# Kernel optimization log

Hardware: AMD Instinct MI355X
Metric: run time of the kernel (lower is better)

Reference implementation:

```python
import jax, jax.numpy as jnp
import numpy as np

EPS_BN = 1e-5
EPS_COS = 1e-8
M_BINS = 10


def _bn(x, g, b):
    # eval-mode BatchNorm2d with running_mean=0, running_var=1
    s = g / jnp.sqrt(1.0 + EPS_BN)
    return x * s[None, :, None, None] + b[None, :, None, None]


def _dw(x, w, pad, dil):
    # depthwise conv, x [B,C,H,W], w [C,1,kh,kw]
    return jax.lax.conv_general_dilated(
        x, w, window_strides=(1, 1), padding=pad, rhs_dilation=dil,
        dimension_numbers=('NCHW', 'OIHW', 'NCHW'),
        feature_group_count=x.shape[1])


def setup_inputs() -> dict:
    key = jax.random.key(0)
    ks = jax.random.split(key, 20)
    B, INP, OUP, H, W = 16, 64, 64, 128, 128
    f32 = jnp.float32
    d = {}
    d['x'] = jax.random.normal(ks[0], (B, INP, H, W), f32)
    d['w_conv1'] = jax.random.normal(ks[1], (OUP, INP), f32) * 0.05
    d['pr_w1'] = jax.random.normal(ks[2], (OUP, 1, 1, 5), f32) * 0.2
    d['pr_w2'] = jax.random.normal(ks[3], (OUP, 1, 5, 1), f32) * 0.2
    d['pr_w3'] = jax.random.normal(ks[4], (OUP, 1, 1, 5), f32) * 0.2
    d['pr_w4'] = jax.random.normal(ks[5], (OUP, 1, 5, 1), f32) * 0.2
    d['pr_gamma'] = 1.0 + 0.1 * jax.random.normal(ks[6], (5, OUP), f32)
    d['pr_beta'] = 0.1 * jax.random.normal(ks[7], (5, OUP), f32)
    d['bn1_g'] = 1.0 + 0.1 * jax.random.normal(ks[8], (OUP,), f32)
    d['bn1_b'] = 0.1 * jax.random.normal(ks[9], (OUP,), f32)
    d['bn2_g'] = 1.0 + 0.1 * jax.random.normal(ks[10], (OUP,), f32)
    d['bn2_b'] = 0.1 * jax.random.normal(ks[11], (OUP,), f32)
    d['fc1_w'] = jax.random.normal(ks[12], (OUP, 2), f32) * 0.5
    d['fc1_b'] = 0.1 * jax.random.normal(ks[13], (OUP,), f32)
    d['phi1_w'] = jax.random.normal(ks[14], (OUP, OUP), f32) * 0.1
    d['phi1_b'] = 0.01 * jax.random.normal(ks[15], (OUP,), f32)
    d['phi2_w'] = jax.random.normal(ks[16], (OUP, OUP), f32) * 0.1
    d['phi2_b'] = 0.01 * jax.random.normal(ks[17], (OUP,), f32)
    d['phi3_w'] = jax.random.normal(ks[18], (OUP, OUP), f32) * 0.1
    d['phi3_b'] = 0.01 * jax.random.normal(ks[19], (OUP,), f32)
    d['w_conv2'] = jax.random.normal(jax.random.fold_in(key, 99), (OUP, 1), f32) * 0.1
    return d


def reference(x, w_conv1, pr_w1, pr_w2, pr_w3, pr_w4, pr_gamma, pr_beta,
              bn1_g, bn1_b, bn2_g, bn2_b, fc1_w, fc1_b,
              phi1_w, phi1_b, phi2_w, phi2_b, phi3_w, phi3_b, w_conv2):
    B, C, H, W = x.shape
    M = M_BINS
    OUP = w_conv1.shape[0]
    # conv1 (1x1) + Position_reinforcement branch
    x_c = jnp.einsum('oc,bchw->bohw', w_conv1, x)
    h = _bn(x_c, pr_gamma[0], pr_beta[0])
    h = _dw(h, pr_w1, ((0, 0), (2, 2)), (1, 1))
    h = _bn(h, pr_gamma[1], pr_beta[1])
    h = _dw(h, pr_w2, ((2, 2), (0, 0)), (1, 1))
    h = _bn(h, pr_gamma[2], pr_beta[2])
    h = _dw(h, pr_w3, ((0, 0), (4, 4)), (2, 2))
    h = _bn(h, pr_gamma[3], pr_beta[3])
    h = _dw(h, pr_w4, ((4, 4), (0, 0)), (2, 2))
    x_center = _bn(h, pr_gamma[4], pr_beta[4])
    # cosine similarity of each pixel feature with the global-avg feature
    g = jnp.mean(x, axis=(2, 3), keepdims=True)             # [B,C,1,1]
    num = jnp.sum(g * x, axis=1)                            # [B,H,W]
    gn = jnp.maximum(jnp.sqrt(jnp.sum(g * g, axis=1)), EPS_COS)
    xn = jnp.maximum(jnp.sqrt(jnp.sum(x * x, axis=1)), EPS_COS)
    S = num / (gn * xn)                                     # [B,H,W]
    Sf = S.reshape(B, H * W)
    # torch casts min/max with float() -> detached constants
    mn = jax.lax.stop_gradient(jnp.min(Sf, axis=1))
    mx = jax.lax.stop_gradient(jnp.max(Sf, axis=1))
    t = jnp.arange(M, dtype=x.dtype) / (M - 1)
    levels = mn[:, None] + (mx - mn)[:, None] * t[None, :]  # [B,M]
    diff = jnp.abs(levels[:, None, :] - Sf[:, :, None])     # [B,HW,M] soft bins
    V = jnp.where(diff < 0.5 / M, 1.0 - diff, jnp.zeros((), x.dtype))
    colsum = jnp.sum(V, axis=1)                             # [B,M]
    # torch normalizes by V.sum() while only columns 0..j are filled -> cumsum
    denom = jnp.cumsum(colsum, axis=1)
    Ch = jnp.stack([colsum / denom, levels], axis=-1)       # [B,M,2]
    Cf = Ch.reshape(-1, 2) @ fc1_w.T + fc1_b                # [B*M,OUP]
    Cq = Cf.reshape(B, OUP, M)                              # raw view as in torch
    p1 = jnp.einsum('oc,bcm->bom', phi1_w, Cq) + phi1_b[None, :, None]
    p2 = jnp.einsum('oc,bcm->bom', phi2_w, Cq) + phi2_b[None, :, None]
    X = jax.nn.softmax(jnp.einsum('bcm,bcn->bmn', p1, p2), axis=-1)  # [B,M,M]
    p3 = jnp.einsum('oc,bcm->bom', phi3_w, Cq) + phi3_b[None, :, None]
    Lp = jnp.einsum('bcm,bmn->bcn', p3, X)                  # [B,OUP,M]
    Vr = V.reshape(B, M, H * W)                             # raw view as in torch
    R = jnp.einsum('bcm,bmk->bck', Lp, Vr).reshape(B, OUP, H, W)
    x_tex = _bn(R, bn1_g, bn1_b)
    x_full = _bn(w_conv2[:, 0][None, :, None, None] * S[:, None, :, :], bn2_g, bn2_b)
    att = jax.nn.sigmoid(x_full + x_tex + x_center)
    return x * att
```

## Files before the change

kernel.cpp:

```cpp
#include <hip/hip_runtime.h>
#include <hip/hip_bf16.h>
#include <math.h>

#define NB   16
#define NC   64
#define NH   128
#define NW   128
#define NHW  16384
#define NM   10

__global__ __launch_bounds__(256) void k_gmean(const float* __restrict__ x,
                                               double* __restrict__ g) {
    int bc = blockIdx.x;
    const float* xp = x + (size_t)bc * NHW;
    double s = 0.0;
    for (int i = threadIdx.x; i < NHW / 4; i += 256) {
        float4 v = ((const float4*)xp)[i];
        s += (double)v.x + (double)v.y + (double)v.z + (double)v.w;
    }
    for (int off = 32; off; off >>= 1) s += __shfl_down(s, off);
    __shared__ double red[4];
    int wid = threadIdx.x >> 6, lane = threadIdx.x & 63;
    if (lane == 0) red[wid] = s;
    __syncthreads();
    if (threadIdx.x == 0)
        g[bc] = (red[0] + red[1] + red[2] + red[3]) * (1.0 / (double)NHW);
}

__global__ __launch_bounds__(256) void k_misc(const float* __restrict__ W,
                                              const double* __restrict__ g,
                                              float* __restrict__ Wt,
                                              double* __restrict__ gn) {
    if (blockIdx.x == 0) {
        for (int e = threadIdx.x; e < 64 * 64; e += 256) {
            int c = e >> 6, o = e & 63;
            Wt[c * 64 + o] = W[o * 64 + c];
        }
    } else if (threadIdx.x == 0) {
        int b = blockIdx.x - 1;
        const double* gb = g + b * NC;
        double gsq = 0.0;
        for (int c = 0; c < NC; ++c) gsq += gb[c] * gb[c];
        gn[b] = fmax(sqrt(gsq), 1e-8);
    }
}

__global__ __launch_bounds__(512) void k_conv1_S(
        const float* __restrict__ x, const float* __restrict__ Wt,
        const double* __restrict__ g, const double* __restrict__ gn,
        float* __restrict__ xc, double* __restrict__ S) {
    __shared__ __align__(16) float Xs[64 * 256];
    int bid = blockIdx.x;
    int b = bid >> 6, k0 = (bid & 63) * 256;
    int tid = threadIdx.x;
    const float* xb = x + (size_t)b * NC * NHW + k0;

    for (int e = tid; e < 64 * 64; e += 512) {
        int c = e >> 6, p4 = (e & 63) << 2;
        *(float4*)&Xs[c * 256 + p4] =
            *(const float4*)&xb[(size_t)c * NHW + p4];
    }
    __syncthreads();

    if (tid < 256) {
        const double* gb = g + b * NC;
        double num = 0.0, sq = 0.0;
#pragma unroll
        for (int c = 0; c < NC; ++c) {
            double v = (double)Xs[c * 256 + tid];
            num += gb[c] * v;
            sq  += v * v;
        }
        double xn = fmax(sqrt(sq), 1e-8);
        S[(size_t)b * NHW + k0 + tid] = num / (gn[b] * xn);
    }

    int o0 = __builtin_amdgcn_readfirstlane((tid >> 6) * 8);
    int px0 = (tid & 63) * 4;
    float acc[8][4];
#pragma unroll
    for (int i = 0; i < 8; ++i)
#pragma unroll
        for (int j = 0; j < 4; ++j) acc[i][j] = 0.f;

#pragma unroll 4
    for (int c = 0; c < NC; ++c) {
        float4 xa = *(float4*)&Xs[c * 256 + px0];
        const float* wr = Wt + c * 64 + o0;
        float xr[4] = {xa.x, xa.y, xa.z, xa.w};
        float wv[8];
#pragma unroll
        for (int i = 0; i < 8; ++i) wv[i] = wr[i];
#pragma unroll
        for (int i = 0; i < 8; ++i)
#pragma unroll
            for (int j = 0; j < 4; ++j)
                acc[i][j] = fmaf(wv[i], xr[j], acc[i][j]);
    }

    float* xcb = xc + (size_t)b * NC * NHW + k0;
#pragma unroll
    for (int i = 0; i < 8; ++i) {
        float4 s0;
        s0.x = acc[i][0]; s0.y = acc[i][1]; s0.z = acc[i][2]; s0.w = acc[i][3];
        *(float4*)&xcb[(size_t)(o0 + i) * NHW + px0] = s0;
    }
}

__global__ __launch_bounds__(256) void k_chain(
        const double* __restrict__ S,
        const float* __restrict__ fc1w, const float* __restrict__ fc1b,
        const float* __restrict__ ph1w, const float* __restrict__ ph1b,
        const float* __restrict__ ph2w, const float* __restrict__ ph2b,
        const float* __restrict__ ph3w, const float* __restrict__ ph3b,
        double* __restrict__ levelsOut, float* __restrict__ LpOut) {
    int b = blockIdx.x, tid = threadIdx.x;
    const double* Sb = S + b * NHW;

    double mn = 1e300, mx = -1e300;
    for (int i = tid; i < NHW; i += 256) {
        double v = Sb[i];
        mn = fmin(mn, v); mx = fmax(mx, v);
    }
    for (int off = 32; off; off >>= 1) {
        mn = fmin(mn, __shfl_down(mn, off));
        mx = fmax(mx, __shfl_down(mx, off));
    }
    __shared__ double rmn[4], rmx[4];
    int wid = tid >> 6, lane = tid & 63;
    if (lane == 0) { rmn[wid] = mn; rmx[wid] = mx; }
    __syncthreads();
    __shared__ double levS[NM];
    if (tid == 0) {
        double a = fmin(fmin(rmn[0], rmn[1]), fmin(rmn[2], rmn[3]));
        double z = fmax(fmax(rmx[0], rmx[1]), fmax(rmx[2], rmx[3]));
        for (int m = 0; m < NM; ++m) levS[m] = a + (z - a) * ((double)m / 9.0);
    }
    __syncthreads();
    double lv[NM];
#pragma unroll
    for (int m = 0; m < NM; ++m) lv[m] = levS[m];

    double bins[NM];
#pragma unroll
    for (int m = 0; m < NM; ++m) bins[m] = 0.0;
    for (int i = tid; i < NHW; i += 256) {
        double v = Sb[i];
#pragma unroll
        for (int m = 0; m < NM; ++m) {
            double d = fabs(lv[m] - v);
            if (d < 0.05) bins[m] += 1.0 - d;
        }
    }
#pragma unroll
    for (int m = 0; m < NM; ++m)
        for (int off = 32; off; off >>= 1) bins[m] += __shfl_down(bins[m], off);
    __shared__ double wb[4][NM];
    if (lane == 0) {
#pragma unroll
        for (int m = 0; m < NM; ++m) wb[wid][m] = bins[m];
    }
    __syncthreads();
    __shared__ float ratio[NM];
    if (tid == 0) {
        double den = 0.0;
        for (int m = 0; m < NM; ++m) {
            double cs = wb[0][m] + wb[1][m] + wb[2][m] + wb[3][m];
            den += cs;
            ratio[m] = (float)(cs / den);
        }
    }
    __syncthreads();

    __shared__ float CfL[640];
    for (int idx = tid; idx < 640; idx += 256) {
        int rm = idx >> 6, o = idx & 63;
        CfL[idx] = ratio[rm] * fc1w[o*2+0] + (float)levS[rm] * fc1w[o*2+1] + fc1b[o];
    }
    __syncthreads();

    __shared__ float P1[640], P2[640], P3[640];
    for (int idx = tid; idx < 640; idx += 256) {
        int o = idx / 10, m = idx - o * 10;
        float a1 = ph1b[o], a2 = ph2b[o], a3 = ph3b[o];
        for (int c2 = 0; c2 < NC; ++c2) {
            float cq = CfL[c2*10 + m];
            a1 = fmaf(ph1w[o*NC + c2], cq, a1);
            a2 = fmaf(ph2w[o*NC + c2], cq, a2);
            a3 = fmaf(ph3w[o*NC + c2], cq, a3);
        }
        P1[idx] = a1; P2[idx] = a2; P3[idx] = a3;
    }
    __syncthreads();

    __shared__ float XL[100];
    if (tid < 100) {
        int m = tid / 10, n = tid - (tid/10)*10;
        float acc = 0.f;
        for (int c2 = 0; c2 < NC; ++c2)
            acc = fmaf(P1[c2*10 + m], P2[c2*10 + n], acc);
        XL[tid] = acc;
    }
    __syncthreads();
    if (tid < NM) {
        float mxr = XL[tid*10];
        for (int n = 1; n < NM; ++n) mxr = fmaxf(mxr, XL[tid*10 + n]);
        float e[NM], sum = 0.f;
        for (int n = 0; n < NM; ++n) { e[n] = expf(XL[tid*10+n] - mxr); sum += e[n]; }
        for (int n = 0; n < NM; ++n) XL[tid*10+n] = e[n] / sum;
    }
    __syncthreads();

    for (int idx = tid; idx < 640; idx += 256) {
        int c2 = idx / 10, n = idx - (idx/10)*10;
        float acc = 0.f;
#pragma unroll
        for (int m = 0; m < NM; ++m) acc = fmaf(P3[c2*10 + m], XL[m*10 + n], acc);
        LpOut[b*640 + idx] = acc;
    }
    if (tid < NM) levelsOut[b*NM + tid] = levS[tid];
}

__global__ __launch_bounds__(256) void k_vgath(
        const double* __restrict__ S, const double* __restrict__ levels,
        float* __restrict__ vg, float* __restrict__ Sf) {
    int P = blockIdx.x * 256 + threadIdx.x;
    int b = P >> 14, k = P & (NHW - 1);
    __shared__ double levL[NM];
    if (threadIdx.x < NM) levL[threadIdx.x] = levels[b*NM + threadIdx.x];
    __syncthreads();
    const double* Sb = S + (size_t)b * NHW;
    float* vgb = vg + (size_t)b * NM * NHW;
#pragma unroll
    for (int i = 0; i < NM; ++i) {
        int j = i * NHW + k;
        int p = j / 10;
        int m = j - p * 10;
        double d = fabs(levL[m] - Sb[p]);
        vgb[i * NHW + k] = (d < 0.05) ? (float)(1.0 - d) : 0.f;
    }
    Sf[P] = (float)Sb[k];
}

__global__ __launch_bounds__(256) void k_dwfinal(
        const float* __restrict__ xc, const float* __restrict__ x,
        const float* __restrict__ vg, const float* __restrict__ Sf,
        const float* __restrict__ Lp,
        const float* __restrict__ pw1, const float* __restrict__ pw2,
        const float* __restrict__ pw3, const float* __restrict__ pw4,
        const float* __restrict__ gamma, const float* __restrict__ beta,
        const float* __restrict__ bn1g, const float* __restrict__ bn1b,
        const float* __restrict__ bn2g, const float* __restrict__ bn2b,
        const float* __restrict__ wconv2, float* __restrict__ out) {
    int tile = blockIdx.x, c = blockIdx.y, b = blockIdx.z;
    int R0 = (tile >> 1) * 32, C0 = (tile & 1) * 64;
    const float inv = 0.9999950000374997f;
    float s0 = gamma[0*NC+c]*inv, b0 = beta[0*NC+c];
    float s1 = gamma[1*NC+c]*inv, b1 = beta[1*NC+c];
    float s2 = gamma[2*NC+c]*inv, b2 = beta[2*NC+c];
    float s3 = gamma[3*NC+c]*inv, b3 = beta[3*NC+c];
    float s4 = gamma[4*NC+c]*inv, b4 = beta[4*NC+c];
    float w1[5], w2[5], w3[5], w4[5];
#pragma unroll
    for (int q = 0; q < 5; ++q) {
        w1[q] = pw1[c*5+q]; w2[q] = pw2[c*5+q];
        w3[q] = pw3[c*5+q]; w4[q] = pw4[c*5+q];
    }
    float Ac = wconv2[c] * (bn2g[c] * inv);
    float Bc = bn2b[c] + bn1b[c];
    float S1 = bn1g[c] * inv;

    __shared__ __align__(16) float A[44*76];
    __shared__ __align__(16) float Bf[44*72];
    __shared__ float LpL[NM];
    const float* src = xc + ((size_t)(b*NC + c)) * NHW;
    int tid = threadIdx.x;

    if (tid < NM) LpL[tid] = Lp[b*640 + c*10 + tid];

    for (int t = tid; t < 44*19; t += 256) {
        int r = t / 19, g2 = t - r*19;
        int gy = R0 - 6 + r, gx0 = C0 - 6 + 4*g2;
        float4 v = make_float4(0.f, 0.f, 0.f, 0.f);
        bool rowOK = (unsigned)gy < NH;
        if (rowOK) {
            const float* rowp = src + gy*NW;
            if ((unsigned)gx0 <= (unsigned)(NW-4)) {
                v = *(const float4*)(rowp + gx0);
            } else {
                float* pv = (float*)&v;
#pragma unroll
                for (int u = 0; u < 4; ++u) {
                    int gx = gx0 + u;
                    if ((unsigned)gx < NW) pv[u] = rowp[gx];
                }
            }
        }
        float4 w;
        w.x = (rowOK && (unsigned)(gx0+0) < NW) ? fmaf(v.x, s0, b0) : 0.f;
        w.y = (rowOK && (unsigned)(gx0+1) < NW) ? fmaf(v.y, s0, b0) : 0.f;
        w.z = (rowOK && (unsigned)(gx0+2) < NW) ? fmaf(v.z, s0, b0) : 0.f;
        w.w = (rowOK && (unsigned)(gx0+3) < NW) ? fmaf(v.w, s0, b0) : 0.f;
        *(float4*)&A[r*76 + 4*g2] = w;
    }
    __syncthreads();

    for (int t = tid; t < 44*18; t += 256) {
        int r = t / 18, g2 = t - r*18;
        float xw[8];
        *(float4*)&xw[0] = *(float4*)&A[r*76 + 4*g2];
        *(float4*)&xw[4] = *(float4*)&A[r*76 + 4*g2 + 4];
        int gy = R0 - 6 + r;
        bool rowOK = (unsigned)gy < NH;
        float o[4];
#pragma unroll
        for (int u = 0; u < 4; ++u) {
            float acc = 0.f;
#pragma unroll
            for (int q = 0; q < 5; ++q) acc = fmaf(w1[q], xw[u+q], acc);
            int gx = C0 - 4 + 4*g2 + u;
            o[u] = (rowOK && (unsigned)gx < NW) ? fmaf(acc, s1, b1) : 0.f;
        }
        *(float4*)&Bf[r*72 + 4*g2] = *(float4*)o;
    }
    __syncthreads();

    for (int t = tid; t < 40*18; t += 256) {
        int r = t / 18, g2 = t - r*18;
        float ys[5][4];
#pragma unroll
        for (int p = 0; p < 5; ++p)
            *(float4*)&ys[p][0] = *(float4*)&Bf[(r+p)*72 + 4*g2];
        int gy = R0 - 4 + r;
        bool rowOK = (unsigned)gy < NH;
        float o[4];
#pragma unroll
        for (int u = 0; u < 4; ++u) {
            float acc = 0.f;
#pragma unroll
            for (int p = 0; p < 5; ++p) acc = fmaf(w2[p], ys[p][u], acc);
            int gx = C0 - 4 + 4*g2 + u;
            o[u] = (rowOK && (unsigned)gx < NW) ? fmaf(acc, s2, b2) : 0.f;
        }
        *(float4*)&A[r*72 + 4*g2] = *(float4*)o;
    }
    __syncthreads();

    for (int t = tid; t < 40*16; t += 256) {
        int r = t >> 4, g2 = t & 15;
        float xw[12];
        *(float4*)&xw[0] = *(float4*)&A[r*72 + 4*g2];
        *(float4*)&xw[4] = *(float4*)&A[r*72 + 4*g2 + 4];
        *(float4*)&xw[8] = *(float4*)&A[r*72 + 4*g2 + 8];
        int gy = R0 - 4 + r;
        bool rowOK = (unsigned)gy < NH;
        float o[4];
#pragma unroll
        for (int u = 0; u < 4; ++u) {
            float acc = 0.f;
#pragma unroll
            for (int q = 0; q < 5; ++q) acc = fmaf(w3[q], xw[u+2*q], acc);
            o[u] = rowOK ? fmaf(acc, s3, b3) : 0.f;
        }
        *(float4*)&Bf[r*64 + 4*g2] = *(float4*)o;
    }
    __syncthreads();

    const float* vgb = vg + (size_t)b * NM * NHW;
    const float* Sfb = Sf + (size_t)b * NHW;
    for (int t = tid; t < 32*16; t += 256) {
        int r = t >> 4, g2 = t & 15;
        float ys[5][4];
#pragma unroll
        for (int p = 0; p < 5; ++p)
            *(float4*)&ys[p][0] = *(float4*)&Bf[(r+2*p)*64 + 4*g2];
        int kbase = (R0 + r) * NW + C0 + 4*g2;
        size_t xbase = (size_t)(b*NC + c) * NHW + kbase;
        float4 xv = *(const float4*)&x[xbase];
        float4 skv = *(const float4*)&Sfb[kbase];
        const float* xvp = (const float*)&xv;
        const float* skp = (const float*)&skv;
        float vr[NM][4];
#pragma unroll
        for (int i = 0; i < NM; ++i)
            *(float4*)&vr[i][0] = *(const float4*)&vgb[i * NHW + kbase];
        float res[4];
#pragma unroll
        for (int u = 0; u < 4; ++u) {
            float acc = 0.f;
#pragma unroll
            for (int p = 0; p < 5; ++p) acc = fmaf(w4[p], ys[p][u], acc);
            float xcen = fmaf(acc, s4, b4);
            float R = 0.f;
#pragma unroll
            for (int i = 0; i < NM; ++i) R = fmaf(LpL[i], vr[i][u], R);
            float pre = fmaf(Ac, skp[u], Bc) + S1 * R + xcen;
            float att = 1.0f / (1.0f + expf(-pre));
            res[u] = xvp[u] * att;
        }
        *(float4*)&out[xbase] = *(float4*)res;
    }
}

extern "C" void kernel_launch(void* const* d_in, const int* in_sizes, int n_in,
                              void* d_out, int out_size, void* d_ws, size_t ws_size,
                              hipStream_t stream) {
    (void)in_sizes; (void)n_in; (void)out_size; (void)ws_size;
    const float* x      = (const float*)d_in[0];
    const float* wconv1 = (const float*)d_in[1];
    const float* pw1    = (const float*)d_in[2];
    const float* pw2    = (const float*)d_in[3];
    const float* pw3    = (const float*)d_in[4];
    const float* pw4    = (const float*)d_in[5];
    const float* pgam   = (const float*)d_in[6];
    const float* pbet   = (const float*)d_in[7];
    const float* bn1g   = (const float*)d_in[8];
    const float* bn1b   = (const float*)d_in[9];
    const float* bn2g   = (const float*)d_in[10];
    const float* bn2b   = (const float*)d_in[11];
    const float* fc1w   = (const float*)d_in[12];
    const float* fc1b   = (const float*)d_in[13];
    const float* ph1w   = (const float*)d_in[14];
    const float* ph1b   = (const float*)d_in[15];
    const float* ph2w   = (const float*)d_in[16];
    const float* ph2b   = (const float*)d_in[17];
    const float* ph3w   = (const float*)d_in[18];
    const float* ph3b   = (const float*)d_in[19];
    const float* wconv2 = (const float*)d_in[20];
    float* out = (float*)d_out;

    float*  ws  = (float*)d_ws;
    float*  xc  = ws;
    double* Sd  = (double*)(ws + 16777216);
    double* g   = Sd + NB * NHW;
    double* lev = g + NB * NC;
    double* gn  = lev + NB * NM;
    float*  Lp  = (float*)(gn + NB);
    float*  vg  = Lp + NB * 640;
    float*  Sf  = vg + NB * NM * NHW;
    float*  Wt  = Sf + NB * NHW;

    k_gmean<<<NB * NC, 256, 0, stream>>>(x, g);
    k_misc<<<17, 256, 0, stream>>>(wconv1, g, Wt, gn);
    k_conv1_S<<<NB * NHW / 256, 512, 0, stream>>>(x, Wt, g, gn, xc, Sd);
    k_chain<<<NB, 256, 0, stream>>>(Sd, fc1w, fc1b, ph1w, ph1b, ph2w, ph2b,
                                    ph3w, ph3b, lev, Lp);
    k_vgath<<<NB * NHW / 256, 256, 0, stream>>>(Sd, lev, vg, Sf);
    k_dwfinal<<<dim3(8, NC, NB), 256, 0, stream>>>(
        xc, x, vg, Sf, Lp, pw1, pw2, pw3, pw4, pgam, pbet,
        bn1g, bn1b, bn2g, bn2b, wconv2, out);
}
```

Before: 170.1 us.

## Retile conv1 into smaller blocks and register-block depthwise stencil passes

The pointwise conv1 kernel now uses 256-thread blocks over 128 pixels. Each thread computes 16 output channels for 2 pixels, so the grid doubles and LDS use per block halves, which should raise occupancy. In the depthwise chain, each thread now handles 8 columns or 4 rows per item, reusing stencil inputs loaded from LDS across more outputs. The final vertical pass computes two output rows per thread from shared loaded rows. This cuts redundant LDS reads, at the cost of more registers and some idle threads in the vertical pass.

```diff
diff --git a/kernel.cpp b/kernel.cpp
--- a/kernel.cpp
+++ b/kernel.cpp
@@ -45,29 +45,29 @@
     }
 }
 
-__global__ __launch_bounds__(512) void k_conv1_S(
+__global__ __launch_bounds__(256) void k_conv1_S(
         const float* __restrict__ x, const float* __restrict__ Wt,
         const double* __restrict__ g, const double* __restrict__ gn,
         float* __restrict__ xc, double* __restrict__ S) {
-    __shared__ __align__(16) float Xs[64 * 256];
+    __shared__ __align__(16) float Xs[64 * 128];
     int bid = blockIdx.x;
-    int b = bid >> 6, k0 = (bid & 63) * 256;
+    int b = bid >> 7, k0 = (bid & 127) * 128;
     int tid = threadIdx.x;
     const float* xb = x + (size_t)b * NC * NHW + k0;
 
-    for (int e = tid; e < 64 * 64; e += 512) {
-        int c = e >> 6, p4 = (e & 63) << 2;
-        *(float4*)&Xs[c * 256 + p4] =
+    for (int e = tid; e < 64 * 32; e += 256) {
+        int c = e >> 5, p4 = (e & 31) << 2;
+        *(float4*)&Xs[c * 128 + p4] =
             *(const float4*)&xb[(size_t)c * NHW + p4];
     }
     __syncthreads();
 
-    if (tid < 256) {
+    if (tid < 128) {
         const double* gb = g + b * NC;
         double num = 0.0, sq = 0.0;
 #pragma unroll
         for (int c = 0; c < NC; ++c) {
-            double v = (double)Xs[c * 256 + tid];
+            double v = (double)Xs[c * 128 + tid];
             num += gb[c] * v;
             sq  += v * v;
         }
@@ -76,34 +76,33 @@
     }
 
     int o0 = __builtin_amdgcn_readfirstlane((tid >> 6) * 8);
-    int px0 = (tid & 63) * 4;
-    float acc[8][4];
-#pragma unroll
-    for (int i = 0; i < 8; ++i)
-#pragma unroll
-        for (int j = 0; j < 4; ++j) acc[i][j] = 0.f;
+    int px0 = (tid & 63) * 2;
+    float acc[16][2];
+#pragma unroll
+    for (int i = 0; i < 16; ++i) { acc[i][0] = 0.f; acc[i][1] = 0.f; }
 
 #pragma unroll 4
     for (int c = 0; c < NC; ++c) {
-        float4 xa = *(float4*)&Xs[c * 256 + px0];
+        float2 xa = *(float2*)&Xs[c * 128 + px0];
         const float* wr = Wt + c * 64 + o0;
-        float xr[4] = {xa.x, xa.y, xa.z, xa.w};
-        float wv[8];
+        float wv[16];
 #pragma unroll
         for (int i = 0; i < 8; ++i) wv[i] = wr[i];
 #pragma unroll
-        for (int i = 0; i < 8; ++i)
-#pragma unroll
-            for (int j = 0; j < 4; ++j)
-                acc[i][j] = fmaf(wv[i], xr[j], acc[i][j]);
+        for (int i = 0; i < 8; ++i) wv[8 + i] = wr[32 + i];
+#pragma unroll
+        for (int i = 0; i < 16; ++i) {
+            acc[i][0] = fmaf(wv[i], xa.x, acc[i][0]);
+            acc[i][1] = fmaf(wv[i], xa.y, acc[i][1]);
+        }
     }
 
     float* xcb = xc + (size_t)b * NC * NHW + k0;
 #pragma unroll
-    for (int i = 0; i < 8; ++i) {
-        float4 s0;
-        s0.x = acc[i][0]; s0.y = acc[i][1]; s0.z = acc[i][2]; s0.w = acc[i][3];
-        *(float4*)&xcb[(size_t)(o0 + i) * NHW + px0] = s0;
+    for (int i = 0; i < 16; ++i) {
+        int o = o0 + ((i < 8) ? i : (24 + i));
+        float2 s0; s0.x = acc[i][0]; s0.y = acc[i][1];
+        *(float2*)&xcb[(size_t)o * NHW + px0] = s0;
     }
 }
 
@@ -305,100 +304,115 @@
     }
     __syncthreads();
 
-    for (int t = tid; t < 44*18; t += 256) {
-        int r = t / 18, g2 = t - r*18;
-        float xw[8];
-        *(float4*)&xw[0] = *(float4*)&A[r*76 + 4*g2];
-        *(float4*)&xw[4] = *(float4*)&A[r*76 + 4*g2 + 4];
+    for (int t = tid; t < 44*9; t += 256) {
+        int r = t / 9, gp = t - r*9;
+        float xw[12];
+        *(float4*)&xw[0] = *(float4*)&A[r*76 + 8*gp];
+        *(float4*)&xw[4] = *(float4*)&A[r*76 + 8*gp + 4];
+        *(float4*)&xw[8] = *(float4*)&A[r*76 + 8*gp + 8];
         int gy = R0 - 6 + r;
         bool rowOK = (unsigned)gy < NH;
-        float o[4];
-#pragma unroll
-        for (int u = 0; u < 4; ++u) {
+        float o[8];
+#pragma unroll
+        for (int u = 0; u < 8; ++u) {
             float acc = 0.f;
 #pragma unroll
             for (int q = 0; q < 5; ++q) acc = fmaf(w1[q], xw[u+q], acc);
-            int gx = C0 - 4 + 4*g2 + u;
+            int gx = C0 - 4 + 8*gp + u;
             o[u] = (rowOK && (unsigned)gx < NW) ? fmaf(acc, s1, b1) : 0.f;
         }
-        *(float4*)&Bf[r*72 + 4*g2] = *(float4*)o;
-    }
-    __syncthreads();
-
-    for (int t = tid; t < 40*18; t += 256) {
-        int r = t / 18, g2 = t - r*18;
-        float ys[5][4];
-#pragma unroll
-        for (int p = 0; p < 5; ++p)
-            *(float4*)&ys[p][0] = *(float4*)&Bf[(r+p)*72 + 4*g2];
+        *(float4*)&Bf[r*72 + 8*gp]     = *(float4*)&o[0];
+        *(float4*)&Bf[r*72 + 8*gp + 4] = *(float4*)&o[4];
+    }
+    __syncthreads();
+
+    if (tid < 180) {
+        int rg = tid / 18, g2 = tid - rg*18;
+        float ys[8][4];
+#pragma unroll
+        for (int m = 0; m < 8; ++m)
+            *(float4*)&ys[m][0] = *(float4*)&Bf[(4*rg + m)*72 + 4*g2];
+        bool colOK[4];
+#pragma unroll
+        for (int u = 0; u < 4; ++u)
+            colOK[u] = (unsigned)(C0 - 4 + 4*g2 + u) < NW;
+#pragma unroll
+        for (int rr = 0; rr < 4; ++rr) {
+            int gy = R0 - 4 + 4*rg + rr;
+            bool rowOK = (unsigned)gy < NH;
+            float o[4];
+#pragma unroll
+            for (int u = 0; u < 4; ++u) {
+                float acc = 0.f;
+#pragma unroll
+                for (int p = 0; p < 5; ++p) acc = fmaf(w2[p], ys[rr+p][u], acc);
+                o[u] = (rowOK && colOK[u]) ? fmaf(acc, s2, b2) : 0.f;
+            }
+            *(float4*)&A[(4*rg + rr)*72 + 4*g2] = *(float4*)o;
+        }
+    }
+    __syncthreads();
+
+    for (int t = tid; t < 40*8; t += 256) {
+        int r = t >> 3, gp = t & 7;
+        float xw[16];
+        *(float4*)&xw[0]  = *(float4*)&A[r*72 + 8*gp];
+        *(float4*)&xw[4]  = *(float4*)&A[r*72 + 8*gp + 4];
+        *(float4*)&xw[8]  = *(float4*)&A[r*72 + 8*gp + 8];
+        *(float4*)&xw[12] = *(float4*)&A[r*72 + 8*gp + 12];
         int gy = R0 - 4 + r;
         bool rowOK = (unsigned)gy < NH;
-        float o[4];
-#pragma unroll
-        for (int u = 0; u < 4; ++u) {
-            float acc = 0.f;
-#pragma unroll
-            for (int p = 0; p < 5; ++p) acc = fmaf(w2[p], ys[p][u], acc);
-            int gx = C0 - 4 + 4*g2 + u;
-            o[u] = (rowOK && (unsigned)gx < NW) ? fmaf(acc, s2, b2) : 0.f;
-        }
-        *(float4*)&A[r*72 + 4*g2] = *(float4*)o;
-    }
-    __syncthreads();
-
-    for (int t = tid; t < 40*16; t += 256) {
-        int r = t >> 4, g2 = t & 15;
-        float xw[12];
-        *(float4*)&xw[0] = *(float4*)&A[r*72 + 4*g2];
-        *(float4*)&xw[4] = *(float4*)&A[r*72 + 4*g2 + 4];
-        *(float4*)&xw[8] = *(float4*)&A[r*72 + 4*g2 + 8];
-        int gy = R0 - 4 + r;
-        bool rowOK = (unsigned)gy < NH;
-        float o[4];
-#pragma unroll
-        for (int u = 0; u < 4; ++u) {
+        float o[8];
+#pragma unroll
+        for (int u = 0; u < 8; ++u) {
             float acc = 0.f;
 #pragma unroll
             for (int q = 0; q < 5; ++q) acc = fmaf(w3[q], xw[u+2*q], acc);
             o[u] = rowOK ? fmaf(acc, s3, b3) : 0.f;
         }
-        *(float4*)&Bf[r*64 + 4*g2] = *(float4*)o;
-    }
-    __syncthreads();
-
-    const float* vgb = vg + (size_t)b * NM * NHW;
-    const float* Sfb = Sf + (size_t)b * NHW;
-    for (int t = tid; t < 32*16; t += 256) {
-        int r = t >> 4, g2 = t & 15;
-        float ys[5][4];
-#pragma unroll
-        for (int p = 0; p < 5; ++p)
-            *(float4*)&ys[p][0] = *(float4*)&Bf[(r+2*p)*64 + 4*g2];
-        int kbase = (R0 + r) * NW + C0 + 4*g2;
-        size_t xbase = (size_t)(b*NC + c) * NHW + kbase;
-        float4 xv = *(const float4*)&x[xbase];
-        float4 skv = *(const float4*)&Sfb[kbase];
-        const float* xvp = (const float*)&xv;
-        const float* skp = (const float*)&skv;
-        float vr[NM][4];
-#pragma unroll
-        for (int i = 0; i < NM; ++i)
-            *(float4*)&vr[i][0] = *(const float4*)&vgb[i * NHW + kbase];
-        float res[4];
-#pragma unroll
-        for (int u = 0; u < 4; ++u) {
-            float acc = 0.f;
-#pragma unroll
-            for (int p = 0; p < 5; ++p) acc = fmaf(w4[p], ys[p][u], acc);
-            float xcen = fmaf(acc, s4, b4);
-            float R = 0.f;
-#pragma unroll
-            for (int i = 0; i < NM; ++i) R = fmaf(LpL[i], vr[i][u], R);
-            float pre = fmaf(Ac, skp[u], Bc) + S1 * R + xcen;
-            float att = 1.0f / (1.0f + expf(-pre));
-            res[u] = xvp[u] * att;
-        }
-        *(float4*)&out[xbase] = *(float4*)res;
+        *(float4*)&Bf[r*64 + 8*gp]     = *(float4*)&o[0];
+        *(float4*)&Bf[r*64 + 8*gp + 4] = *(float4*)&o[4];
+    }
+    __syncthreads();
+
+    {
+        int gr = tid >> 4, g2 = tid & 15;
+        int base = (gr & 1) + 4*(gr >> 1);
+        float ys[6][4];
+#pragma unroll
+        for (int m = 0; m < 6; ++m)
+            *(float4*)&ys[m][0] = *(float4*)&Bf[(base + 2*m)*64 + 4*g2];
+        const float* vgb = vg + (size_t)b * NM * NHW;
+        const float* Sfb = Sf + (size_t)b * NHW;
+#pragma unroll
+        for (int j = 0; j < 2; ++j) {
+            int ro = base + 2*j;
+            int kbase = (R0 + ro) * NW + C0 + 4*g2;
+            size_t xbase = (size_t)(b*NC + c) * NHW + kbase;
+            float4 xv = *(const float4*)&x[xbase];
+            float4 skv = *(const float4*)&Sfb[kbase];
+            const float* xvp = (const float*)&xv;
+            const float* skp = (const float*)&skv;
+            float vr[NM][4];
+#pragma unroll
+            for (int i = 0; i < NM; ++i)
+                *(float4*)&vr[i][0] = *(const float4*)&vgb[i * NHW + kbase];
+            float res[4];
+#pragma unroll
+            for (int u = 0; u < 4; ++u) {
+                float acc = 0.f;
+#pragma unroll
+                for (int p = 0; p < 5; ++p) acc = fmaf(w4[p], ys[j+p][u], acc);
+                float xcen = fmaf(acc, s4, b4);
+                float R = 0.f;
+#pragma unroll
+                for (int i = 0; i < NM; ++i) R = fmaf(LpL[i], vr[i][u], R);
+                float pre = fmaf(Ac, skp[u], Bc) + S1 * R + xcen;
+                float att = 1.0f / (1.0f + expf(-pre));
+                res[u] = xvp[u] * att;
+            }
+            *(float4*)&out[xbase] = *(float4*)res;
+        }
     }
 }
 
@@ -442,7 +456,7 @@
 
     k_gmean<<<NB * NC, 256, 0, stream>>>(x, g);
     k_misc<<<17, 256, 0, stream>>>(wconv1, g, Wt, gn);
-    k_conv1_S<<<NB * NHW / 256, 512, 0, stream>>>(x, Wt, g, gn, xc, Sd);
+    k_conv1_S<<<NB * NHW / 128, 256, 0, stream>>>(x, Wt, g, gn, xc, Sd);
     k_chain<<<NB, 256, 0, stream>>>(Sd, fc1w, fc1b, ph1w, ph1b, ph2w, ph2b,
                                     ph3w, ph3b, lev, Lp);
     k_vgath<<<NB * NHW / 256, 256, 0, stream>>>(Sd, lev, vg, Sf);
```

After: 172.9 us. About the same (+1.7%).

## Split min/max and histogram across more blocks; register-resident conv1 per pixel

Applied to the files above, without the earlier changes.

The min/max and soft-histogram reductions move out of the 16-block chain kernel into separate kernels that each use 64 blocks, with per-part partial results combined in the chain kernel. This spreads the serial per-batch reductions over more CUs. The conv1+cosine kernel also drops the shared-memory tile: each thread holds all 64 channels of one pixel in registers and computes 64 outputs in 8 passes, using uniform weight loads. This trades shared-memory traffic for register pressure, adds two kernel launches, and changes the order of the bin summation slightly.

```diff
diff --git a/kernel.cpp b/kernel.cpp
--- a/kernel.cpp
+++ b/kernel.cpp
@@ -45,127 +45,135 @@
     }
 }
 
-__global__ __launch_bounds__(512) void k_conv1_S(
+__global__ __launch_bounds__(256, 4) void k_conv1_S(
         const float* __restrict__ x, const float* __restrict__ Wt,
         const double* __restrict__ g, const double* __restrict__ gn,
         float* __restrict__ xc, double* __restrict__ S) {
-    __shared__ __align__(16) float Xs[64 * 256];
-    int bid = blockIdx.x;
-    int b = bid >> 6, k0 = (bid & 63) * 256;
-    int tid = threadIdx.x;
-    const float* xb = x + (size_t)b * NC * NHW + k0;
-
-    for (int e = tid; e < 64 * 64; e += 512) {
-        int c = e >> 6, p4 = (e & 63) << 2;
-        *(float4*)&Xs[c * 256 + p4] =
-            *(const float4*)&xb[(size_t)c * NHW + p4];
-    }
-    __syncthreads();
-
-    if (tid < 256) {
+    int P = blockIdx.x * 256 + threadIdx.x;
+    int b = P >> 14, k = P & (NHW - 1);
+    const float* xb = x + (size_t)b * NC * NHW + k;
+
+    float xv[NC];
+#pragma unroll
+    for (int c = 0; c < NC; ++c) xv[c] = xb[(size_t)c * NHW];
+
+    {
         const double* gb = g + b * NC;
         double num = 0.0, sq = 0.0;
 #pragma unroll
         for (int c = 0; c < NC; ++c) {
-            double v = (double)Xs[c * 256 + tid];
+            double v = (double)xv[c];
             num += gb[c] * v;
             sq  += v * v;
         }
         double xn = fmax(sqrt(sq), 1e-8);
-        S[(size_t)b * NHW + k0 + tid] = num / (gn[b] * xn);
-    }
-
-    int o0 = __builtin_amdgcn_readfirstlane((tid >> 6) * 8);
-    int px0 = (tid & 63) * 4;
-    float acc[8][4];
-#pragma unroll
-    for (int i = 0; i < 8; ++i)
-#pragma unroll
-        for (int j = 0; j < 4; ++j) acc[i][j] = 0.f;
-
-#pragma unroll 4
-    for (int c = 0; c < NC; ++c) {
-        float4 xa = *(float4*)&Xs[c * 256 + px0];
-        const float* wr = Wt + c * 64 + o0;
-        float xr[4] = {xa.x, xa.y, xa.z, xa.w};
-        float wv[8];
-#pragma unroll
-        for (int i = 0; i < 8; ++i) wv[i] = wr[i];
-#pragma unroll
-        for (int i = 0; i < 8; ++i)
-#pragma unroll
-            for (int j = 0; j < 4; ++j)
-                acc[i][j] = fmaf(wv[i], xr[j], acc[i][j]);
-    }
-
-    float* xcb = xc + (size_t)b * NC * NHW + k0;
-#pragma unroll
-    for (int i = 0; i < 8; ++i) {
-        float4 s0;
-        s0.x = acc[i][0]; s0.y = acc[i][1]; s0.z = acc[i][2]; s0.w = acc[i][3];
-        *(float4*)&xcb[(size_t)(o0 + i) * NHW + px0] = s0;
+        S[P] = num / (gn[b] * xn);
+    }
+
+    float* xcb = xc + (size_t)b * NC * NHW + k;
+    for (int p = 0; p < 8; ++p) {
+        int o0 = p * 8;
+        float acc[8];
+#pragma unroll
+        for (int j = 0; j < 8; ++j) acc[j] = 0.f;
+#pragma unroll
+        for (int c = 0; c < NC; ++c) {
+            const float* wr = Wt + c * 64 + o0;
+#pragma unroll
+            for (int j = 0; j < 8; ++j)
+                acc[j] = fmaf(wr[j], xv[c], acc[j]);
+        }
+#pragma unroll
+        for (int j = 0; j < 8; ++j)
+            xcb[(size_t)(o0 + j) * NHW] = acc[j];
+    }
+}
+
+__global__ __launch_bounds__(256) void k_minmax(const double* __restrict__ S,
+                                                double* __restrict__ pmn,
+                                                double* __restrict__ pmx) {
+    int blk = blockIdx.x, b = blk >> 2, part = blk & 3;
+    const double* Sb = S + (size_t)b * NHW + part * 4096;
+    int tid = threadIdx.x;
+    double mn = 1e300, mx = -1e300;
+    for (int i = tid; i < 4096; i += 256) {
+        double v = Sb[i];
+        mn = fmin(mn, v); mx = fmax(mx, v);
+    }
+    for (int off = 32; off; off >>= 1) {
+        mn = fmin(mn, __shfl_down(mn, off));
+        mx = fmax(mx, __shfl_down(mx, off));
+    }
+    __shared__ double rmn[4], rmx[4];
+    int wid = tid >> 6, lane = tid & 63;
+    if (lane == 0) { rmn[wid] = mn; rmx[wid] = mx; }
+    __syncthreads();
+    if (tid == 0) {
+        pmn[blk] = fmin(fmin(rmn[0], rmn[1]), fmin(rmn[2], rmn[3]));
+        pmx[blk] = fmax(fmax(rmx[0], rmx[1]), fmax(rmx[2], rmx[3]));
+    }
+}
+
+__global__ __launch_bounds__(256) void k_hist(const double* __restrict__ S,
+                                              const double* __restrict__ pmn,
+                                              const double* __restrict__ pmx,
+                                              double* __restrict__ pbins) {
+    int blk = blockIdx.x, b = blk >> 2, part = blk & 3;
+    double a = fmin(fmin(pmn[4*b], pmn[4*b+1]), fmin(pmn[4*b+2], pmn[4*b+3]));
+    double z = fmax(fmax(pmx[4*b], pmx[4*b+1]), fmax(pmx[4*b+2], pmx[4*b+3]));
+    double lv[NM];
+#pragma unroll
+    for (int m = 0; m < NM; ++m) lv[m] = a + (z - a) * ((double)m / 9.0);
+
+    const double* Sb = S + (size_t)b * NHW + part * 4096;
+    int tid = threadIdx.x;
+    double bins[NM];
+#pragma unroll
+    for (int m = 0; m < NM; ++m) bins[m] = 0.0;
+    for (int i = tid; i < 4096; i += 256) {
+        double v = Sb[i];
+#pragma unroll
+        for (int m = 0; m < NM; ++m) {
+            double d = fabs(lv[m] - v);
+            if (d < 0.05) bins[m] += 1.0 - d;
+        }
+    }
+#pragma unroll
+    for (int m = 0; m < NM; ++m)
+        for (int off = 32; off; off >>= 1) bins[m] += __shfl_down(bins[m], off);
+    __shared__ double wb[4][NM];
+    int wid = tid >> 6, lane = tid & 63;
+    if (lane == 0) {
+#pragma unroll
+        for (int m = 0; m < NM; ++m) wb[wid][m] = bins[m];
+    }
+    __syncthreads();
+    if (tid == 0) {
+#pragma unroll
+        for (int m = 0; m < NM; ++m)
+            pbins[blk * NM + m] = wb[0][m] + wb[1][m] + wb[2][m] + wb[3][m];
     }
 }
 
 __global__ __launch_bounds__(256) void k_chain(
-        const double* __restrict__ S,
+        const double* __restrict__ pmn, const double* __restrict__ pmx,
+        const double* __restrict__ pbins,
         const float* __restrict__ fc1w, const float* __restrict__ fc1b,
         const float* __restrict__ ph1w, const float* __restrict__ ph1b,
         const float* __restrict__ ph2w, const float* __restrict__ ph2b,
         const float* __restrict__ ph3w, const float* __restrict__ ph3b,
         double* __restrict__ levelsOut, float* __restrict__ LpOut) {
     int b = blockIdx.x, tid = threadIdx.x;
-    const double* Sb = S + b * NHW;
-
-    double mn = 1e300, mx = -1e300;
-    for (int i = tid; i < NHW; i += 256) {
-        double v = Sb[i];
-        mn = fmin(mn, v); mx = fmax(mx, v);
-    }
-    for (int off = 32; off; off >>= 1) {
-        mn = fmin(mn, __shfl_down(mn, off));
-        mx = fmax(mx, __shfl_down(mx, off));
-    }
-    __shared__ double rmn[4], rmx[4];
-    int wid = tid >> 6, lane = tid & 63;
-    if (lane == 0) { rmn[wid] = mn; rmx[wid] = mx; }
-    __syncthreads();
     __shared__ double levS[NM];
-    if (tid == 0) {
-        double a = fmin(fmin(rmn[0], rmn[1]), fmin(rmn[2], rmn[3]));
-        double z = fmax(fmax(rmx[0], rmx[1]), fmax(rmx[2], rmx[3]));
-        for (int m = 0; m < NM; ++m) levS[m] = a + (z - a) * ((double)m / 9.0);
-    }
-    __syncthreads();
-    double lv[NM];
-#pragma unroll
-    for (int m = 0; m < NM; ++m) lv[m] = levS[m];
-
-    double bins[NM];
-#pragma unroll
-    for (int m = 0; m < NM; ++m) bins[m] = 0.0;
-    for (int i = tid; i < NHW; i += 256) {
-        double v = Sb[i];
-#pragma unroll
-        for (int m = 0; m < NM; ++m) {
-            double d = fabs(lv[m] - v);
-            if (d < 0.05) bins[m] += 1.0 - d;
-        }
-    }
-#pragma unroll
-    for (int m = 0; m < NM; ++m)
-        for (int off = 32; off; off >>= 1) bins[m] += __shfl_down(bins[m], off);
-    __shared__ double wb[4][NM];
-    if (lane == 0) {
-#pragma unroll
-        for (int m = 0; m < NM; ++m) wb[wid][m] = bins[m];
-    }
-    __syncthreads();
     __shared__ float ratio[NM];
     if (tid == 0) {
+        double a = fmin(fmin(pmn[4*b], pmn[4*b+1]), fmin(pmn[4*b+2], pmn[4*b+3]));
+        double z = fmax(fmax(pmx[4*b], pmx[4*b+1]), fmax(pmx[4*b+2], pmx[4*b+3]));
+        for (int m = 0; m < NM; ++m) levS[m] = a + (z - a) * ((double)m / 9.0);
         double den = 0.0;
         for (int m = 0; m < NM; ++m) {
-            double cs = wb[0][m] + wb[1][m] + wb[2][m] + wb[3][m];
+            double cs = ((pbins[(4*b)*NM+m] + pbins[(4*b+1)*NM+m])
+                        + pbins[(4*b+2)*NM+m]) + pbins[(4*b+3)*NM+m];
             den += cs;
             ratio[m] = (float)(cs / den);
         }
@@ -429,22 +437,28 @@
     const float* wconv2 = (const float*)d_in[20];
     float* out = (float*)d_out;
 
-    float*  ws  = (float*)d_ws;
-    float*  xc  = ws;
-    double* Sd  = (double*)(ws + 16777216);
-    double* g   = Sd + NB * NHW;
-    double* lev = g + NB * NC;
-    double* gn  = lev + NB * NM;
-    float*  Lp  = (float*)(gn + NB);
-    float*  vg  = Lp + NB * 640;
-    float*  Sf  = vg + NB * NM * NHW;
-    float*  Wt  = Sf + NB * NHW;
+    float*  ws    = (float*)d_ws;
+    float*  xc    = ws;
+    double* Sd    = (double*)(ws + 16777216);
+    double* g     = Sd + NB * NHW;
+    double* lev   = g + NB * NC;
+    double* gn    = lev + NB * NM;
+    double* pmn   = gn + NB;
+    double* pmx   = pmn + 64;
+    double* pbins = pmx + 64;
+    float*  Lp    = (float*)(pbins + 640);
+    float*  vg    = Lp + NB * 640;
+    float*  Sf    = vg + NB * NM * NHW;
+    float*  Wt    = Sf + NB * NHW;
 
     k_gmean<<<NB * NC, 256, 0, stream>>>(x, g);
     k_misc<<<17, 256, 0, stream>>>(wconv1, g, Wt, gn);
-    k_conv1_S<<<NB * NHW / 256, 512, 0, stream>>>(x, Wt, g, gn, xc, Sd);
-    k_chain<<<NB, 256, 0, stream>>>(Sd, fc1w, fc1b, ph1w, ph1b, ph2w, ph2b,
-                                    ph3w, ph3b, lev, Lp);
+    k_conv1_S<<<NB * NHW / 256, 256, 0, stream>>>(x, Wt, g, gn, xc, Sd);
+    k_minmax<<<NB * 4, 256, 0, stream>>>(Sd, pmn, pmx);
+    k_hist<<<NB * 4, 256, 0, stream>>>(Sd, pmn, pmx, pbins);
+    k_chain<<<NB, 256, 0, stream>>>(pmn, pmx, pbins, fc1w, fc1b,
+                                    ph1w, ph1b, ph2w, ph2b, ph3w, ph3b,
+                                    lev, Lp);
     k_vgath<<<NB * NHW / 256, 256, 0, stream>>>(Sd, lev, vg, Sf);
     k_dwfinal<<<dim3(8, NC, NB), 256, 0, stream>>>(
         xc, x, vg, Sf, Lp, pw1, pw2, pw3, pw4, pgam, pbet,
```

After: 159.4 us. 6.3% less time.
